# Kernel tuning notes

Measured on AMD Instinct MI355X. Metric: run time of the kernel, lower is better.

## Reference

```python
import jax, jax.numpy as jnp
import numpy as np

N, P, E, IN = 50000, 4, 500000, 128   # nodes, metapaths, edges/metapath, in_size
H, F = 8, 32                           # num_heads, out_feats per head (hidden_size)
HF = H * F                             # flattened embedding (256)
HS = 128                               # semantic attention hidden size
B, OUT = 128, 2                        # num contracts (graphs), classes
NEG_SLOPE = 0.2                        # DGL GATConv LeakyReLU slope


def setup_inputs() -> dict:
    key = jax.random.key(0)
    ks = jax.random.split(key, 14)
    return {
        "h": jax.random.normal(ks[0], (N, IN), jnp.float32),
        "Wg": jax.random.normal(ks[1], (P, IN, HF), jnp.float32) * 0.1,
        "attn_l": jax.random.normal(ks[2], (P, H, F), jnp.float32) * 0.1,
        "attn_r": jax.random.normal(ks[3], (P, H, F), jnp.float32) * 0.1,
        "gat_bias": jax.random.normal(ks[4], (P, HF), jnp.float32) * 0.1,
        "sem_W1": jax.random.normal(ks[5], (HF, HS), jnp.float32) * 0.1,
        "sem_b1": jax.random.normal(ks[6], (HS,), jnp.float32) * 0.1,
        "sem_W2": jax.random.normal(ks[7], (HS, 1), jnp.float32) * 0.1,
        "cls_W": jax.random.normal(ks[8], (HF, OUT), jnp.float32) * 0.1,
        "cls_b": jax.random.normal(ks[9], (OUT,), jnp.float32) * 0.1,
        "src": jax.random.randint(ks[10], (P, E), 0, N, jnp.int32),
        "dst": jax.random.randint(ks[11], (P, E), 0, N, jnp.int32),
        "graph_ids": jax.random.randint(ks[12], (N,), 0, B, jnp.int32),
    }


def _gat(h, W, al, ar, bias, s, d):
    """One DGL-style GATConv over an edge list (dropout=identity, eval mode)."""
    n = h.shape[0]
    hp = (h @ W).reshape(n, H, F)                 # [N,H,F] projected features
    el = (hp * al).sum(-1)                        # [N,H] src attention term
    er = (hp * ar).sum(-1)                        # [N,H] dst attention term
    e = jax.nn.leaky_relu(el[s] + er[d], NEG_SLOPE)        # [E,H] edge scores
    m = jax.ops.segment_max(e, d, num_segments=n)          # per-dst max (softmax stab.)
    a = jnp.exp(e - m[d])                                  # [E,H]
    den = jax.ops.segment_sum(a, d, num_segments=n)        # [N,H]
    alpha = a / den[d]                                     # edge softmax over in-neighbors
    out = jax.ops.segment_sum(alpha[:, :, None] * hp[s], d, num_segments=n)  # [N,H,F]
    return jax.nn.elu(out + bias.reshape(1, H, F)).reshape(n, HF)


def reference(h, Wg, attn_l, attn_r, gat_bias, sem_W1, sem_b1, sem_W2,
              cls_W, cls_b, src, dst, graph_ids):
    n = h.shape[0]
    # GATConv per meta-path (small fixed loop over P=4 metapaths)
    embs = [_gat(h, Wg[p], attn_l[p], attn_r[p], gat_bias[p], src[p], dst[p])
            for p in range(Wg.shape[0])]
    z = jnp.stack(embs, axis=1)                   # [N,P,HF]
    # Semantic attention over meta-paths
    w = jnp.tanh(z @ sem_W1 + sem_b1) @ sem_W2    # [N,P,1]
    beta = jax.nn.softmax(w.mean(0), axis=0)      # [P,1]
    fused = (beta[None] * z).sum(1)               # [N,HF]
    # Per-graph (filename) mean pooling
    seg = jax.ops.segment_sum(fused, graph_ids, num_segments=B)
    cnt = jax.ops.segment_sum(jnp.ones((n,), fused.dtype), graph_ids, num_segments=B)
    pooled = seg / jnp.maximum(cnt, 1.0)[:, None]  # [B,HF]
    logits = pooled @ cls_W + cls_b                # [B,OUT]
    return (logits, pooled)
```

## Files before the change

### kernel.cpp

```cpp
#include <hip/hip_runtime.h>

#define NN 50000
#define PM 4
#define EE 500000
#define INF_ 128
#define NH 8
#define FF 32
#define HF 256
#define HS 128
#define BG 128
#define OUTC 2

#define NB2 98
#define BCAP 6144
#define BCH 4096
#define GCAP 576
#define NBG2 782

typedef __attribute__((ext_vector_type(8))) short bf16x8;
typedef __attribute__((ext_vector_type(4))) float f32x4;

__device__ __forceinline__ float b2f(unsigned short x) {
  unsigned u = ((unsigned)x) << 16;
  return __builtin_bit_cast(float, u);
}
__device__ __forceinline__ unsigned short f2b(float f) {
  unsigned u = __builtin_bit_cast(unsigned, f);
  u += 0x7fff + ((u >> 16) & 1);
  return (unsigned short)(u >> 16);
}
__device__ __forceinline__ float fexp(float x) { return __expf(x); }
__device__ __forceinline__ float ftanh(float x) {
  float t = __expf(-2.f * fabsf(x));
  float r = (1.f - t) / (1.f + t);
  return copysignf(r, x);
}

__global__ __launch_bounds__(256) void prep_kernel(
    const float* __restrict__ h, const float* __restrict__ Wg,
    const float* __restrict__ W1, const float* __restrict__ al,
    const float* __restrict__ ar,
    unsigned short* __restrict__ h_b, unsigned short* __restrict__ Wb_t,
    unsigned short* __restrict__ W1_t, float* __restrict__ wl,
    float* __restrict__ wr, int* __restrict__ gcnt, int* __restrict__ gcnt2) {
  int b = blockIdx.x;
  int tid = threadIdx.x;
  if (b < 1) {
    for (int i = tid; i < PM * NB2; i += 256) gcnt[i] = 0;
    if (tid < BG) gcnt2[tid] = 0;
    return;
  }
  b -= 1;
  if (b < 6250) {
    int t = b * 256 + tid;
    float4 v = *(const float4*)(h + (size_t)t * 4);
    ushort4 o;
    o.x = f2b(v.x); o.y = f2b(v.y); o.z = f2b(v.z); o.w = f2b(v.w);
    *(ushort4*)(h_b + (size_t)t * 4) = o;
    return;
  }
  b -= 6250;
  if (b < 512) {
    int t = b * 256 + tid;
    int p = t >> 15, rem = t & 32767;
    int n = rem >> 7, k = rem & 127;
    Wb_t[(size_t)p * 32768 + n * 128 + k] = f2b(Wg[(size_t)p * 32768 + k * 256 + n]);
    return;
  }
  b -= 512;
  if (b < 128) {
    int t = b * 256 + tid;
    int n = t >> 8, k = t & 255;
    W1_t[n * 256 + k] = f2b(W1[k * 128 + n]);
    return;
  }
  b -= 128;
  {
    int t = b * 256 + tid;
    int p = t >> 10, rem = t & 1023;
    int k = rem >> 3, hh = rem & 7;
    const float* wrow = Wg + (size_t)p * 32768 + k * 256 + hh * 32;
    const float* alp = al + p * 256 + hh * 32;
    const float* arp = ar + p * 256 + hh * 32;
    float sl = 0.f, sr = 0.f;
    #pragma unroll
    for (int f = 0; f < 32; f++) { sl += wrow[f] * alp[f]; sr += wrow[f] * arp[f]; }
    wl[t] = sl; wr[t] = sr;
  }
}

__global__ __launch_bounds__(256) void bucket_kernel(
    const int* __restrict__ src, const int* __restrict__ dst,
    unsigned* __restrict__ bdata, int* __restrict__ gcnt) {
  __shared__ unsigned ed[BCH];
  __shared__ int hist[NB2], gbase[NB2], cur[NB2];
  int p = blockIdx.y;
  int e0 = blockIdx.x * BCH;
  int n = min(BCH, EE - e0);
  int tid = threadIdx.x;
  if (tid < NB2) hist[tid] = 0;
  __syncthreads();
  const int* sp = src + (size_t)p * EE + e0;
  const int* dp = dst + (size_t)p * EE + e0;
  for (int i = tid; i < n; i += 256) {
    int s = sp[i], d = dp[i];
    ed[i] = ((unsigned)d << 16) | (unsigned)s;
    atomicAdd(&hist[d >> 9], 1);
  }
  __syncthreads();
  if (tid < NB2) {
    gbase[tid] = atomicAdd(&gcnt[p * NB2 + tid], hist[tid]);
    cur[tid] = 0;
  }
  __syncthreads();
  for (int i = tid; i < n; i += 256) {
    unsigned pk = ed[i];
    int bk = pk >> 25;
    int slot = gbase[bk] + atomicAdd(&cur[bk], 1);
    if (slot < BCAP)
      bdata[((size_t)(p * NB2 + bk)) * BCAP + slot] = pk;
  }
}

__global__ __launch_bounds__(256) void gbucket_kernel(
    const int* __restrict__ gid, int* __restrict__ glist, int* __restrict__ gcnt2) {
  __shared__ int gl[BCH];
  __shared__ int hist[BG], gbase[BG], cur[BG];
  int e0 = blockIdx.x * BCH;
  int n = min(BCH, NN - e0);
  int tid = threadIdx.x;
  if (tid < BG) hist[tid] = 0;
  __syncthreads();
  for (int i = tid; i < n; i += 256) {
    int g = gid[e0 + i];
    gl[i] = g;
    atomicAdd(&hist[g], 1);
  }
  __syncthreads();
  if (tid < BG) {
    gbase[tid] = atomicAdd(&gcnt2[tid], hist[tid]);
    cur[tid] = 0;
  }
  __syncthreads();
  for (int i = tid; i < n; i += 256) {
    int g = gl[i];
    int slot = gbase[g] + atomicAdd(&cur[g], 1);
    if (slot < GCAP) glist[g * GCAP + slot] = e0 + i;
  }
}

__global__ __launch_bounds__(256) void csrify_kernel(
    const unsigned* __restrict__ bdata, const int* __restrict__ gcnt,
    int* __restrict__ off, unsigned short* __restrict__ csr) {
  __shared__ unsigned ebuf[BCAP];
  __shared__ int gc[NB2];
  __shared__ int degc[512];
  __shared__ int loff[513];
  __shared__ int tmp[256];
  __shared__ int base_s;
  int b = blockIdx.x, p = blockIdx.y;
  int tid = threadIdx.x;
  if (tid < NB2) gc[tid] = min(gcnt[p * NB2 + tid], BCAP);
  __syncthreads();
  if (tid == 0) {
    int s = 0;
    for (int i = 0; i < b; i++) s += gc[i];
    base_s = s;
  }
  int cnt = gc[b];
  const unsigned* bp = bdata + ((size_t)(p * NB2 + b)) * BCAP;
  for (int i = tid; i < cnt; i += 256) ebuf[i] = bp[i];
  degc[tid] = 0; degc[256 + tid] = 0;
  __syncthreads();
  for (int i = tid; i < cnt; i += 256)
    atomicAdd(&degc[(ebuf[i] >> 16) & 511], 1);
  __syncthreads();
  int d0 = degc[2 * tid], d1 = degc[2 * tid + 1];
  tmp[tid] = d0 + d1;
  __syncthreads();
  for (int o = 1; o < 256; o <<= 1) {
    int v = (tid >= o) ? tmp[tid - o] : 0;
    __syncthreads();
    tmp[tid] += v;
    __syncthreads();
  }
  int bse = tmp[tid] - d0 - d1;
  loff[2 * tid] = bse; loff[2 * tid + 1] = bse + d0;
  if (tid == 255) loff[512] = tmp[255];
  __syncthreads();
  int base = base_s;
  for (int dl = tid; dl < 512; dl += 256) {
    int n = b * 512 + dl;
    if (n <= NN) off[(size_t)p * (NN + 1) + n] = base + loff[dl];
  }
  degc[tid] = 0; degc[256 + tid] = 0;
  __syncthreads();
  for (int i = tid; i < cnt; i += 256) {
    unsigned pk = ebuf[i];
    int dl = (pk >> 16) & 511;
    int slot = loff[dl] + atomicAdd(&degc[dl], 1);
    csr[(size_t)p * EE + base + slot] = (unsigned short)(pk & 0xffff);
  }
}

__global__ __launch_bounds__(256) void gemm1_kernel(
    const unsigned short* __restrict__ hA, const unsigned short* __restrict__ Bt,
    unsigned short* __restrict__ Cb, int M, int p0, size_t cstride) {
  __shared__ unsigned short As[64 * 128];
  __shared__ unsigned short Bs[128 * 128];
  int tid = threadIdx.x;
  int pl = blockIdx.z;
  const unsigned short* Bp = Bt + (size_t)(p0 + pl) * 32768;
  unsigned short* Cp = Cb + (size_t)pl * cstride;
  int row0 = blockIdx.x * 64, col0 = blockIdx.y * 128;
  #pragma unroll
  for (int i = 0; i < 4; i++) {
    int c = i * 256 + tid;
    int row = c >> 4, g = c & 15;
    int grow = row0 + row;
    uint4 v = make_uint4(0, 0, 0, 0);
    if (grow < M) v = *(const uint4*)(hA + (size_t)grow * 128 + g * 8);
    *(uint4*)&As[row * 128 + ((g ^ (row & 15)) << 3)] = v;
  }
  #pragma unroll
  for (int i = 0; i < 8; i++) {
    int c = i * 256 + tid;
    int row = c >> 4, g = c & 15;
    uint4 v = *(const uint4*)(Bp + (size_t)(col0 + row) * 128 + g * 8);
    *(uint4*)&Bs[row * 128 + ((g ^ (row & 15)) << 3)] = v;
  }
  __syncthreads();
  int wave = tid >> 6, lane = tid & 63;
  int ln = lane & 15, quad = lane >> 4;
  int mbase = (wave >> 1) * 32, nbase = (wave & 1) * 64;
  f32x4 acc[2][4] = {};
  #pragma unroll
  for (int ks = 0; ks < 4; ks++) {
    int g = ks * 4 + quad;
    bf16x8 a[2], bb[4];
    #pragma unroll
    for (int mi = 0; mi < 2; mi++) {
      int r = mbase + mi * 16 + ln;
      a[mi] = *(const bf16x8*)&As[r * 128 + ((g ^ ln) << 3)];
    }
    #pragma unroll
    for (int ni = 0; ni < 4; ni++) {
      int r = nbase + ni * 16 + ln;
      bb[ni] = *(const bf16x8*)&Bs[r * 128 + ((g ^ ln) << 3)];
    }
    #pragma unroll
    for (int mi = 0; mi < 2; mi++)
      #pragma unroll
      for (int ni = 0; ni < 4; ni++)
        acc[mi][ni] = __builtin_amdgcn_mfma_f32_16x16x32_bf16(a[mi], bb[ni], acc[mi][ni], 0, 0, 0);
  }
  #pragma unroll
  for (int mi = 0; mi < 2; mi++) {
    int gm0 = row0 + mbase + mi * 16 + quad * 4;
    #pragma unroll
    for (int ni = 0; ni < 4; ni++) {
      int gn = col0 + nbase + ni * 16 + ln;
      #pragma unroll
      for (int r = 0; r < 4; r++) {
        int gm = gm0 + r;
        if (gm < M) Cp[(size_t)gm * 256 + gn] = f2b(acc[mi][ni][r]);
      }
    }
  }
}

__global__ __launch_bounds__(256) void elr_kernel(
    const unsigned short* __restrict__ h_b, const float* __restrict__ wl,
    const float* __restrict__ wr, float* __restrict__ el,
    float* __restrict__ er, int N, int p0, size_t estride) {
  __shared__ float wls[128 * 8], wrs[128 * 8];
  int pl = blockIdx.y;
  const float* wlp = wl + (size_t)(p0 + pl) * 1024;
  const float* wrp = wr + (size_t)(p0 + pl) * 1024;
  float* elp = el + (size_t)pl * estride;
  float* erp = er + (size_t)pl * estride;
  for (int i = threadIdx.x; i < 1024; i += 256) { wls[i] = wlp[i]; wrs[i] = wrp[i]; }
  __syncthreads();
  int n = blockIdx.x * 256 + threadIdx.x;
  if (n >= N) return;
  float accl[8] = {}, accr[8] = {};
  for (int kk = 0; kk < 16; kk++) {
    uint4 raw = *(const uint4*)(h_b + (size_t)n * 128 + kk * 8);
    unsigned uu[4] = {raw.x, raw.y, raw.z, raw.w};
    #pragma unroll
    for (int q = 0; q < 4; q++) {
      float v0 = __builtin_bit_cast(float, uu[q] << 16);
      float v1 = __builtin_bit_cast(float, uu[q] & 0xffff0000u);
      int k = kk * 8 + q * 2;
      #pragma unroll
      for (int hh = 0; hh < 8; hh++) {
        accl[hh] += v0 * wls[k * 8 + hh] + v1 * wls[(k + 1) * 8 + hh];
        accr[hh] += v0 * wrs[k * 8 + hh] + v1 * wrs[(k + 1) * 8 + hh];
      }
    }
  }
  *(float4*)(elp + (size_t)n * 8)     = make_float4(accl[0], accl[1], accl[2], accl[3]);
  *(float4*)(elp + (size_t)n * 8 + 4) = make_float4(accl[4], accl[5], accl[6], accl[7]);
  *(float4*)(erp + (size_t)n * 8)     = make_float4(accr[0], accr[1], accr[2], accr[3]);
  *(float4*)(erp + (size_t)n * 8 + 4) = make_float4(accr[4], accr[5], accr[6], accr[7]);
}

__global__ __launch_bounds__(256) void agg_kernel(
    const unsigned short* __restrict__ hp_b, const float* __restrict__ el,
    const float* __restrict__ er, const unsigned short* __restrict__ csr,
    const int* __restrict__ off, const float* __restrict__ bias,
    unsigned short* __restrict__ emb_b, int N, int p0,
    size_t hstride, size_t estride, size_t embstride) {
  int pl = blockIdx.y;
  int p = p0 + pl;
  const unsigned short* hp = hp_b + (size_t)pl * hstride;
  const float* elp = el + (size_t)pl * estride;
  const float* erp = er + (size_t)pl * estride;
  const unsigned short* csrp = csr + (size_t)p * EE;
  const int* offp = off + (size_t)p * (NN + 1);
  const float* bp = bias + (size_t)p * HF;
  unsigned short* embp = emb_b + (size_t)pl * embstride;
  int n = blockIdx.x * 4 + (threadIdx.x >> 6);
  if (n >= N) return;
  int lane = threadIdx.x & 63;
  int h = lane >> 3;
  int e0 = offp[n], e1 = offp[n + 1];
  float erh = erp[n * NH + h];
  float den = 0.f, a0 = 0.f, a1 = 0.f, a2 = 0.f, a3 = 0.f;
  int e = e0;
  for (; e + 8 <= e1; e += 8) {
    int s[8];
    #pragma unroll
    for (int j = 0; j < 8; j++) s[j] = csrp[e + j];
    float x[8];
    #pragma unroll
    for (int j = 0; j < 8; j++) x[j] = elp[s[j] * NH + h];
    ushort4 hv[8];
    #pragma unroll
    for (int j = 0; j < 8; j++)
      hv[j] = *(const ushort4*)(hp + (size_t)s[j] * HF + lane * 4);
    float w[8];
    #pragma unroll
    for (int j = 0; j < 8; j++) {
      float xx = x[j] + erh;
      xx = fmaxf(xx, 0.2f * xx);
      w[j] = fexp(xx);
    }
    den += ((w[0] + w[1]) + (w[2] + w[3])) + ((w[4] + w[5]) + (w[6] + w[7]));
    a0 += ((w[0] * b2f(hv[0].x) + w[1] * b2f(hv[1].x)) + (w[2] * b2f(hv[2].x) + w[3] * b2f(hv[3].x)))
        + ((w[4] * b2f(hv[4].x) + w[5] * b2f(hv[5].x)) + (w[6] * b2f(hv[6].x) + w[7] * b2f(hv[7].x)));
    a1 += ((w[0] * b2f(hv[0].y) + w[1] * b2f(hv[1].y)) + (w[2] * b2f(hv[2].y) + w[3] * b2f(hv[3].y)))
        + ((w[4] * b2f(hv[4].y) + w[5] * b2f(hv[5].y)) + (w[6] * b2f(hv[6].y) + w[7] * b2f(hv[7].y)));
    a2 += ((w[0] * b2f(hv[0].z) + w[1] * b2f(hv[1].z)) + (w[2] * b2f(hv[2].z) + w[3] * b2f(hv[3].z)))
        + ((w[4] * b2f(hv[4].z) + w[5] * b2f(hv[5].z)) + (w[6] * b2f(hv[6].z) + w[7] * b2f(hv[7].z)));
    a3 += ((w[0] * b2f(hv[0].w) + w[1] * b2f(hv[1].w)) + (w[2] * b2f(hv[2].w) + w[3] * b2f(hv[3].w)))
        + ((w[4] * b2f(hv[4].w) + w[5] * b2f(hv[5].w)) + (w[6] * b2f(hv[6].w) + w[7] * b2f(hv[7].w)));
  }
  if (e + 4 <= e1) {
    int s0 = csrp[e], s1 = csrp[e + 1], s2 = csrp[e + 2], s3 = csrp[e + 3];
    float x0 = elp[s0 * NH + h] + erh;
    float x1 = elp[s1 * NH + h] + erh;
    float x2 = elp[s2 * NH + h] + erh;
    float x3 = elp[s3 * NH + h] + erh;
    ushort4 h0 = *(const ushort4*)(hp + (size_t)s0 * HF + lane * 4);
    ushort4 h1 = *(const ushort4*)(hp + (size_t)s1 * HF + lane * 4);
    ushort4 h2 = *(const ushort4*)(hp + (size_t)s2 * HF + lane * 4);
    ushort4 h3 = *(const ushort4*)(hp + (size_t)s3 * HF + lane * 4);
    x0 = fmaxf(x0, 0.2f * x0); x1 = fmaxf(x1, 0.2f * x1);
    x2 = fmaxf(x2, 0.2f * x2); x3 = fmaxf(x3, 0.2f * x3);
    float w0 = fexp(x0), w1 = fexp(x1), w2 = fexp(x2), w3 = fexp(x3);
    den += (w0 + w1) + (w2 + w3);
    a0 += (w0 * b2f(h0.x) + w1 * b2f(h1.x)) + (w2 * b2f(h2.x) + w3 * b2f(h3.x));
    a1 += (w0 * b2f(h0.y) + w1 * b2f(h1.y)) + (w2 * b2f(h2.y) + w3 * b2f(h3.y));
    a2 += (w0 * b2f(h0.z) + w1 * b2f(h1.z)) + (w2 * b2f(h2.z) + w3 * b2f(h3.z));
    a3 += (w0 * b2f(h0.w) + w1 * b2f(h1.w)) + (w2 * b2f(h2.w) + w3 * b2f(h3.w));
    e += 4;
  }
  for (; e < e1; e++) {
    int s = csrp[e];
    float x = elp[s * NH + h] + erh;
    x = fmaxf(x, 0.2f * x);
    float w = fexp(x);
    den += w;
    ushort4 hv = *(const ushort4*)(hp + (size_t)s * HF + lane * 4);
    a0 += w * b2f(hv.x); a1 += w * b2f(hv.y);
    a2 += w * b2f(hv.z); a3 += w * b2f(hv.w);
  }
  float inv = (den > 0.f) ? 1.f / den : 0.f;
  float4 bv = *(const float4*)(bp + lane * 4);
  float o0 = a0 * inv + bv.x, o1 = a1 * inv + bv.y;
  float o2 = a2 * inv + bv.z, o3 = a3 * inv + bv.w;
  o0 = (o0 > 0.f) ? o0 : fexp(o0) - 1.f;
  o1 = (o1 > 0.f) ? o1 : fexp(o1) - 1.f;
  o2 = (o2 > 0.f) ? o2 : fexp(o2) - 1.f;
  o3 = (o3 > 0.f) ? o3 : fexp(o3) - 1.f;
  ushort4 ov;
  ov.x = f2b(o0); ov.y = f2b(o1); ov.z = f2b(o2); ov.w = f2b(o3);
  *(ushort4*)(embp + (size_t)n * HF + lane * 4) = ov;
}

__global__ __launch_bounds__(256) void gemm2_kernel(
    const unsigned short* __restrict__ A, const unsigned short* __restrict__ Bt,
    const float* __restrict__ b1, const float* __restrict__ W2,
    float* __restrict__ wpart, int M, int p0, size_t astride) {
  __shared__ unsigned short As[64 * 128];
  __shared__ unsigned short Bs[128 * 128];
  __shared__ float wred[4];
  int tid = threadIdx.x;
  int pl = blockIdx.y;
  const unsigned short* Ap = A + (size_t)pl * astride;
  int row0 = blockIdx.x * 64;
  int wave = tid >> 6, lane = tid & 63;
  int ln = lane & 15, quad = lane >> 4;
  int mbase = (wave >> 1) * 32, nbase = (wave & 1) * 64;
  f32x4 acc[2][4] = {};
  for (int kc = 0; kc < 2; kc++) {
    #pragma unroll
    for (int i = 0; i < 4; i++) {
      int c = i * 256 + tid;
      int row = c >> 4, g = c & 15;
      int grow = row0 + row;
      uint4 v = make_uint4(0, 0, 0, 0);
      if (grow < M) v = *(const uint4*)(Ap + (size_t)grow * 256 + kc * 128 + g * 8);
      *(uint4*)&As[row * 128 + ((g ^ (row & 15)) << 3)] = v;
    }
    #pragma unroll
    for (int i = 0; i < 8; i++) {
      int c = i * 256 + tid;
      int row = c >> 4, g = c & 15;
      uint4 v = *(const uint4*)(Bt + (size_t)row * 256 + kc * 128 + g * 8);
      *(uint4*)&Bs[row * 128 + ((g ^ (row & 15)) << 3)] = v;
    }
    __syncthreads();
    #pragma unroll
    for (int ks = 0; ks < 4; ks++) {
      int g = ks * 4 + quad;
      bf16x8 a[2], bb[4];
      #pragma unroll
      for (int mi = 0; mi < 2; mi++) {
        int r = mbase + mi * 16 + ln;
        a[mi] = *(const bf16x8*)&As[r * 128 + ((g ^ ln) << 3)];
      }
      #pragma unroll
      for (int ni = 0; ni < 4; ni++) {
        int r = nbase + ni * 16 + ln;
        bb[ni] = *(const bf16x8*)&Bs[r * 128 + ((g ^ ln) << 3)];
      }
      #pragma unroll
      for (int mi = 0; mi < 2; mi++)
        #pragma unroll
        for (int ni = 0; ni < 4; ni++)
          acc[mi][ni] = __builtin_amdgcn_mfma_f32_16x16x32_bf16(a[mi], bb[ni], acc[mi][ni], 0, 0, 0);
    }
    __syncthreads();
  }
  float b1v[4], w2v[4];
  #pragma unroll
  for (int ni = 0; ni < 4; ni++) {
    int col = nbase + ni * 16 + ln;
    b1v[ni] = b1[col]; w2v[ni] = W2[col];
  }
  float s = 0.f;
  #pragma unroll
  for (int mi = 0; mi < 2; mi++) {
    int gm0 = row0 + mbase + mi * 16 + quad * 4;
    #pragma unroll
    for (int r = 0; r < 4; r++) {
      if (gm0 + r < M) {
        #pragma unroll
        for (int ni = 0; ni < 4; ni++)
          s += ftanh(acc[mi][ni][r] + b1v[ni]) * w2v[ni];
      }
    }
  }
  #pragma unroll
  for (int o = 32; o > 0; o >>= 1) s += __shfl_down(s, o);
  if (lane == 0) wred[wave] = s;
  __syncthreads();
  if (tid == 0)
    wpart[(size_t)(p0 + pl) * NBG2 + blockIdx.x] =
        (wred[0] + wred[1]) + (wred[2] + wred[3]);
}

__global__ __launch_bounds__(256) void pool_kernel(
    const unsigned short* __restrict__ emb, const int* __restrict__ glist,
    const int* __restrict__ gcnt2, float* __restrict__ pool,
    int p0, size_t embstride) {
  __shared__ int nl[GCAP];
  __shared__ float sm[4][64][4];
  int b = blockIdx.x, pl = blockIdx.y;
  const unsigned short* embp = emb + (size_t)pl * embstride;
  int tid = threadIdx.x;
  int cnt = min(gcnt2[b], GCAP);
  for (int i = tid; i < cnt; i += 256) nl[i] = glist[b * GCAP + i];
  __syncthreads();
  int sub = tid >> 6, lane = tid & 63;
  float a0 = 0.f, a1 = 0.f, a2 = 0.f, a3 = 0.f;
  for (int i = sub; i < cnt; i += 4) {
    ushort4 v = *(const ushort4*)(embp + (size_t)nl[i] * HF + lane * 4);
    a0 += b2f(v.x); a1 += b2f(v.y); a2 += b2f(v.z); a3 += b2f(v.w);
  }
  sm[sub][lane][0] = a0; sm[sub][lane][1] = a1;
  sm[sub][lane][2] = a2; sm[sub][lane][3] = a3;
  __syncthreads();
  int fl = tid >> 2, j = tid & 3;
  float s = sm[0][fl][j] + sm[1][fl][j] + sm[2][fl][j] + sm[3][fl][j];
  pool[((size_t)(p0 + pl) * BG + b) * HF + tid] = s;
}

__global__ __launch_bounds__(256) void final_kernel(
    const float* __restrict__ pool, const float* __restrict__ wpart,
    const int* __restrict__ gcnt2, const float* __restrict__ clsW,
    const float* __restrict__ clsb, float* __restrict__ out, int N) {
  int b = blockIdx.x;
  int f = threadIdx.x;
  __shared__ float red[256];
  float wm[PM];
  #pragma unroll
  for (int p = 0; p < PM; p++) {
    float s = 0.f;
    for (int i = f; i < NBG2; i += 256) s += wpart[(size_t)p * NBG2 + i];
    red[f] = s;
    __syncthreads();
    for (int st = 128; st > 0; st >>= 1) {
      if (f < st) red[f] += red[f + st];
      __syncthreads();
    }
    wm[p] = red[0] / (float)N;
    __syncthreads();
  }
  float c = fmaxf((float)gcnt2[b], 1.f);
  float mx = -1e30f;
  #pragma unroll
  for (int p = 0; p < PM; p++) mx = fmaxf(mx, wm[p]);
  float es = 0.f, e[PM];
  #pragma unroll
  for (int p = 0; p < PM; p++) { e[p] = expf(wm[p] - mx); es += e[p]; }
  float v = 0.f;
  #pragma unroll
  for (int p = 0; p < PM; p++)
    v += (e[p] / es) * pool[((size_t)p * BG + b) * HF + f];
  v /= c;
  out[256 + (size_t)b * HF + f] = v;
  __shared__ float sm[256];
  sm[f] = v * clsW[f * 2 + 0];
  __syncthreads();
  for (int st = 128; st > 0; st >>= 1) {
    if (f < st) sm[f] += sm[f + st];
    __syncthreads();
  }
  float l0 = sm[0];
  __syncthreads();
  sm[f] = v * clsW[f * 2 + 1];
  __syncthreads();
  for (int st = 128; st > 0; st >>= 1) {
    if (f < st) sm[f] += sm[f + st];
    __syncthreads();
  }
  if (f == 0) {
    out[b * 2 + 0] = l0 + clsb[0];
    out[b * 2 + 1] = sm[0] + clsb[1];
  }
}

extern "C" void kernel_launch(void* const* d_in, const int* in_sizes, int n_in,
                              void* d_out, int out_size, void* d_ws, size_t ws_size,
                              hipStream_t stream) {
  const float* h      = (const float*)d_in[0];
  const float* Wg     = (const float*)d_in[1];
  const float* attn_l = (const float*)d_in[2];
  const float* attn_r = (const float*)d_in[3];
  const float* gatb   = (const float*)d_in[4];
  const float* semW1  = (const float*)d_in[5];
  const float* semb1  = (const float*)d_in[6];
  const float* semW2  = (const float*)d_in[7];
  const float* clsW   = (const float*)d_in[8];
  const float* clsb   = (const float*)d_in[9];
  const int*   src    = (const int*)d_in[10];
  const int*   dst    = (const int*)d_in[11];
  const int*   gid    = (const int*)d_in[12];
  float* out = (float*)d_out;

  auto layout_size = [](int PMg) -> size_t {
    size_t o = 0;
    auto alloc = [&](size_t bytes) { o += (bytes + 255) & ~(size_t)255; };
    alloc((size_t)NN * INF_ * 2);
    alloc((size_t)PMg * NN * HF * 2);
    alloc((size_t)PMg * NN * HF * 2);
    alloc((size_t)PM * HF * INF_ * 2);
    alloc((size_t)HS * HF * 2);
    alloc((size_t)PM * INF_ * NH * 4);
    alloc((size_t)PM * INF_ * NH * 4);
    alloc((size_t)PMg * NN * NH * 4);
    alloc((size_t)PMg * NN * NH * 4);
    alloc((size_t)PM * NB2 * BCAP * 4);
    alloc((size_t)PM * NB2 * 4);
    alloc((size_t)BG * GCAP * 4);
    alloc((size_t)BG * 4);
    alloc((size_t)PM * (NN + 1) * 4);
    alloc((size_t)PM * EE * 2);
    alloc((size_t)PM * BG * HF * 4);
    alloc((size_t)PM * NBG2 * 4);
    return o;
  };
  int PMg = (layout_size(4) <= ws_size) ? 4 : 1;

  char* ws = (char*)d_ws;
  size_t o = 0;
  auto alloc = [&](size_t bytes) { size_t r = o; o += (bytes + 255) & ~(size_t)255; return r; };
  unsigned short* h_b   = (unsigned short*)(ws + alloc((size_t)NN * INF_ * 2));
  unsigned short* hp_b  = (unsigned short*)(ws + alloc((size_t)PMg * NN * HF * 2));
  unsigned short* emb_b = (unsigned short*)(ws + alloc((size_t)PMg * NN * HF * 2));
  unsigned short* Wb_t  = (unsigned short*)(ws + alloc((size_t)PM * HF * INF_ * 2));
  unsigned short* W1_t  = (unsigned short*)(ws + alloc((size_t)HS * HF * 2));
  float* wl    = (float*)(ws + alloc((size_t)PM * INF_ * NH * 4));
  float* wr    = (float*)(ws + alloc((size_t)PM * INF_ * NH * 4));
  float* el    = (float*)(ws + alloc((size_t)PMg * NN * NH * 4));
  float* er    = (float*)(ws + alloc((size_t)PMg * NN * NH * 4));
  unsigned* bdata = (unsigned*)(ws + alloc((size_t)PM * NB2 * BCAP * 4));
  int*   gcnt  = (int*)(ws + alloc((size_t)PM * NB2 * 4));
  int*   glist = (int*)(ws + alloc((size_t)BG * GCAP * 4));
  int*   gcnt2 = (int*)(ws + alloc((size_t)BG * 4));
  int*   off   = (int*)(ws + alloc((size_t)PM * (NN + 1) * 4));
  unsigned short* csr = (unsigned short*)(ws + alloc((size_t)PM * EE * 2));
  float* pool  = (float*)(ws + alloc((size_t)PM * BG * HF * 4));
  float* wpart = (float*)(ws + alloc((size_t)PM * NBG2 * 4));

  const size_t hpS  = (PMg == 4) ? (size_t)NN * HF : 0;
  const size_t embS = hpS;
  const size_t elS  = (PMg == 4) ? (size_t)NN * NH : 0;

  prep_kernel<<<1 + 6250 + 512 + 128 + 16, 256, 0, stream>>>(
      h, Wg, semW1, attn_l, attn_r, h_b, Wb_t, W1_t, wl, wr, gcnt, gcnt2);
  bucket_kernel<<<dim3((EE + BCH - 1) / BCH, PM), 256, 0, stream>>>(src, dst, bdata, gcnt);
  gbucket_kernel<<<(NN + BCH - 1) / BCH, 256, 0, stream>>>(gid, glist, gcnt2);
  csrify_kernel<<<dim3(NB2, PM), 256, 0, stream>>>(bdata, gcnt, off, csr);

  if (PMg == 4) {
    gemm1_kernel<<<dim3((NN + 63) / 64, 2, 4), 256, 0, stream>>>(h_b, Wb_t, hp_b, NN, 0, hpS);
    elr_kernel<<<dim3((NN + 255) / 256, 4), 256, 0, stream>>>(h_b, wl, wr, el, er, NN, 0, elS);
    agg_kernel<<<dim3((NN + 3) / 4, 4), 256, 0, stream>>>(
        hp_b, el, er, csr, off, gatb, emb_b, NN, 0, hpS, elS, embS);
    gemm2_kernel<<<dim3(NBG2, 4), 256, 0, stream>>>(
        emb_b, W1_t, semb1, semW2, wpart, NN, 0, embS);
    pool_kernel<<<dim3(BG, 4), 256, 0, stream>>>(emb_b, glist, gcnt2, pool, 0, embS);
  } else {
    for (int p = 0; p < PM; p++) {
      gemm1_kernel<<<dim3((NN + 63) / 64, 2, 1), 256, 0, stream>>>(h_b, Wb_t, hp_b, NN, p, 0);
      elr_kernel<<<dim3((NN + 255) / 256, 1), 256, 0, stream>>>(h_b, wl, wr, el, er, NN, p, 0);
      agg_kernel<<<dim3((NN + 3) / 4, 1), 256, 0, stream>>>(
          hp_b, el, er, csr, off, gatb, emb_b, NN, p, 0, 0, 0);
      gemm2_kernel<<<dim3(NBG2, 1), 256, 0, stream>>>(
          emb_b, W1_t, semb1, semW2, wpart, NN, p, 0);
      pool_kernel<<<dim3(BG, 1), 256, 0, stream>>>(emb_b, glist, gcnt2, pool, p, 0);
    }
  }

  final_kernel<<<BG, 256, 0, stream>>>(pool, wpart, gcnt2, clsW, clsb, out, NN);
}
```

Before: 457.2 us.

## Merge independent kernels into combined launches and reuse A fragments across metapaths

Merges independent kernel pairs into single launches, with each block choosing its role from its block index: edge bucketing with graph bucketing, GEMM1 with the el/er projection, and GEMM2 with pooling. The GEMM1 blocks now loop over all metapaths, loading the h tile and its MFMA A fragments once and reusing them, instead of using a z grid dimension. This removes several launch gaps, lets the small kernels fill idle compute units, and cuts repeated A loads. In exchange, GEMM1 has fewer blocks each doing more sequential work, and the shared shared-memory size may limit occupancy for the lighter roles.

```diff
diff --git a/kernel.cpp b/kernel.cpp
--- a/kernel.cpp
+++ b/kernel.cpp
@@ -14,7 +14,11 @@
 #define NB2 98
 #define BCAP 6144
 #define BCH 4096
+#define NBB 123
+#define NGB 13
 #define GCAP 576
+#define NBG1 782
+#define NBE 196
 #define NBG2 782
 
 typedef __attribute__((ext_vector_type(8))) short bf16x8;
@@ -89,63 +93,70 @@
   }
 }
 
-__global__ __launch_bounds__(256) void bucket_kernel(
+__global__ __launch_bounds__(256) void bg_kernel(
     const int* __restrict__ src, const int* __restrict__ dst,
-    unsigned* __restrict__ bdata, int* __restrict__ gcnt) {
-  __shared__ unsigned ed[BCH];
-  __shared__ int hist[NB2], gbase[NB2], cur[NB2];
-  int p = blockIdx.y;
-  int e0 = blockIdx.x * BCH;
-  int n = min(BCH, EE - e0);
+    unsigned* __restrict__ bdata, int* __restrict__ gcnt,
+    const int* __restrict__ gid, int* __restrict__ glist,
+    int* __restrict__ gcnt2) {
+  __shared__ __align__(16) char smem[18432];
+  int b = blockIdx.x;
   int tid = threadIdx.x;
-  if (tid < NB2) hist[tid] = 0;
-  __syncthreads();
-  const int* sp = src + (size_t)p * EE + e0;
-  const int* dp = dst + (size_t)p * EE + e0;
-  for (int i = tid; i < n; i += 256) {
-    int s = sp[i], d = dp[i];
-    ed[i] = ((unsigned)d << 16) | (unsigned)s;
-    atomicAdd(&hist[d >> 9], 1);
-  }
-  __syncthreads();
-  if (tid < NB2) {
-    gbase[tid] = atomicAdd(&gcnt[p * NB2 + tid], hist[tid]);
-    cur[tid] = 0;
-  }
-  __syncthreads();
-  for (int i = tid; i < n; i += 256) {
-    unsigned pk = ed[i];
-    int bk = pk >> 25;
-    int slot = gbase[bk] + atomicAdd(&cur[bk], 1);
-    if (slot < BCAP)
-      bdata[((size_t)(p * NB2 + bk)) * BCAP + slot] = pk;
-  }
-}
-
-__global__ __launch_bounds__(256) void gbucket_kernel(
-    const int* __restrict__ gid, int* __restrict__ glist, int* __restrict__ gcnt2) {
-  __shared__ int gl[BCH];
-  __shared__ int hist[BG], gbase[BG], cur[BG];
-  int e0 = blockIdx.x * BCH;
-  int n = min(BCH, NN - e0);
-  int tid = threadIdx.x;
-  if (tid < BG) hist[tid] = 0;
-  __syncthreads();
-  for (int i = tid; i < n; i += 256) {
-    int g = gid[e0 + i];
-    gl[i] = g;
-    atomicAdd(&hist[g], 1);
-  }
-  __syncthreads();
-  if (tid < BG) {
-    gbase[tid] = atomicAdd(&gcnt2[tid], hist[tid]);
-    cur[tid] = 0;
-  }
-  __syncthreads();
-  for (int i = tid; i < n; i += 256) {
-    int g = gl[i];
-    int slot = gbase[g] + atomicAdd(&cur[g], 1);
-    if (slot < GCAP) glist[g * GCAP + slot] = e0 + i;
+  if (b < NBB * PM) {
+    unsigned* ed = (unsigned*)smem;
+    int* hist  = (int*)(smem + BCH * 4);
+    int* gbase = hist + NB2;
+    int* cur   = gbase + NB2;
+    int p = b / NBB, blk = b % NBB;
+    int e0 = blk * BCH;
+    int n = min(BCH, EE - e0);
+    if (tid < NB2) hist[tid] = 0;
+    __syncthreads();
+    const int* sp = src + (size_t)p * EE + e0;
+    const int* dp = dst + (size_t)p * EE + e0;
+    for (int i = tid; i < n; i += 256) {
+      int s = sp[i], d = dp[i];
+      ed[i] = ((unsigned)d << 16) | (unsigned)s;
+      atomicAdd(&hist[d >> 9], 1);
+    }
+    __syncthreads();
+    if (tid < NB2) {
+      gbase[tid] = atomicAdd(&gcnt[p * NB2 + tid], hist[tid]);
+      cur[tid] = 0;
+    }
+    __syncthreads();
+    for (int i = tid; i < n; i += 256) {
+      unsigned pk = ed[i];
+      int bk = pk >> 25;
+      int slot = gbase[bk] + atomicAdd(&cur[bk], 1);
+      if (slot < BCAP)
+        bdata[((size_t)(p * NB2 + bk)) * BCAP + slot] = pk;
+    }
+  } else {
+    int* gl    = (int*)smem;
+    int* hist  = (int*)(smem + BCH * 4);
+    int* gbase = hist + BG;
+    int* cur   = gbase + BG;
+    int blk = b - NBB * PM;
+    int e0 = blk * BCH;
+    int n = min(BCH, NN - e0);
+    if (tid < BG) hist[tid] = 0;
+    __syncthreads();
+    for (int i = tid; i < n; i += 256) {
+      int g = gid[e0 + i];
+      gl[i] = g;
+      atomicAdd(&hist[g], 1);
+    }
+    __syncthreads();
+    if (tid < BG) {
+      gbase[tid] = atomicAdd(&gcnt2[tid], hist[tid]);
+      cur[tid] = 0;
+    }
+    __syncthreads();
+    for (int i = tid; i < n; i += 256) {
+      int g = gl[i];
+      int slot = gbase[g] + atomicAdd(&cur[g], 1);
+      if (slot < GCAP) glist[g * GCAP + slot] = e0 + i;
+    }
   }
 }
 
@@ -203,106 +214,121 @@
   }
 }
 
-__global__ __launch_bounds__(256) void gemm1_kernel(
+__global__ __launch_bounds__(256) void g1elr_kernel(
     const unsigned short* __restrict__ hA, const unsigned short* __restrict__ Bt,
-    unsigned short* __restrict__ Cb, int M, int p0, size_t cstride) {
-  __shared__ unsigned short As[64 * 128];
-  __shared__ unsigned short Bs[128 * 128];
+    unsigned short* __restrict__ Cb, const float* __restrict__ wl,
+    const float* __restrict__ wr, float* __restrict__ el, float* __restrict__ er,
+    int M, int p0, int npaths, size_t cstride, size_t estride) {
+  __shared__ __align__(16) char smem[49152];
+  int b = blockIdx.x;
   int tid = threadIdx.x;
-  int pl = blockIdx.z;
-  const unsigned short* Bp = Bt + (size_t)(p0 + pl) * 32768;
-  unsigned short* Cp = Cb + (size_t)pl * cstride;
-  int row0 = blockIdx.x * 64, col0 = blockIdx.y * 128;
-  #pragma unroll
-  for (int i = 0; i < 4; i++) {
-    int c = i * 256 + tid;
-    int row = c >> 4, g = c & 15;
-    int grow = row0 + row;
-    uint4 v = make_uint4(0, 0, 0, 0);
-    if (grow < M) v = *(const uint4*)(hA + (size_t)grow * 128 + g * 8);
-    *(uint4*)&As[row * 128 + ((g ^ (row & 15)) << 3)] = v;
-  }
-  #pragma unroll
-  for (int i = 0; i < 8; i++) {
-    int c = i * 256 + tid;
-    int row = c >> 4, g = c & 15;
-    uint4 v = *(const uint4*)(Bp + (size_t)(col0 + row) * 128 + g * 8);
-    *(uint4*)&Bs[row * 128 + ((g ^ (row & 15)) << 3)] = v;
-  }
-  __syncthreads();
-  int wave = tid >> 6, lane = tid & 63;
-  int ln = lane & 15, quad = lane >> 4;
-  int mbase = (wave >> 1) * 32, nbase = (wave & 1) * 64;
-  f32x4 acc[2][4] = {};
-  #pragma unroll
-  for (int ks = 0; ks < 4; ks++) {
-    int g = ks * 4 + quad;
-    bf16x8 a[2], bb[4];
-    #pragma unroll
-    for (int mi = 0; mi < 2; mi++) {
-      int r = mbase + mi * 16 + ln;
-      a[mi] = *(const bf16x8*)&As[r * 128 + ((g ^ ln) << 3)];
-    }
-    #pragma unroll
-    for (int ni = 0; ni < 4; ni++) {
-      int r = nbase + ni * 16 + ln;
-      bb[ni] = *(const bf16x8*)&Bs[r * 128 + ((g ^ ln) << 3)];
-    }
-    #pragma unroll
-    for (int mi = 0; mi < 2; mi++)
-      #pragma unroll
-      for (int ni = 0; ni < 4; ni++)
-        acc[mi][ni] = __builtin_amdgcn_mfma_f32_16x16x32_bf16(a[mi], bb[ni], acc[mi][ni], 0, 0, 0);
-  }
-  #pragma unroll
-  for (int mi = 0; mi < 2; mi++) {
-    int gm0 = row0 + mbase + mi * 16 + quad * 4;
-    #pragma unroll
-    for (int ni = 0; ni < 4; ni++) {
-      int gn = col0 + nbase + ni * 16 + ln;
-      #pragma unroll
-      for (int r = 0; r < 4; r++) {
-        int gm = gm0 + r;
-        if (gm < M) Cp[(size_t)gm * 256 + gn] = f2b(acc[mi][ni][r]);
-      }
-    }
-  }
-}
-
-__global__ __launch_bounds__(256) void elr_kernel(
-    const unsigned short* __restrict__ h_b, const float* __restrict__ wl,
-    const float* __restrict__ wr, float* __restrict__ el,
-    float* __restrict__ er, int N, int p0, size_t estride) {
-  __shared__ float wls[128 * 8], wrs[128 * 8];
-  int pl = blockIdx.y;
-  const float* wlp = wl + (size_t)(p0 + pl) * 1024;
-  const float* wrp = wr + (size_t)(p0 + pl) * 1024;
-  float* elp = el + (size_t)pl * estride;
-  float* erp = er + (size_t)pl * estride;
-  for (int i = threadIdx.x; i < 1024; i += 256) { wls[i] = wlp[i]; wrs[i] = wrp[i]; }
-  __syncthreads();
-  int n = blockIdx.x * 256 + threadIdx.x;
-  if (n >= N) return;
-  float accl[8] = {}, accr[8] = {};
-  for (int kk = 0; kk < 16; kk++) {
-    uint4 raw = *(const uint4*)(h_b + (size_t)n * 128 + kk * 8);
-    unsigned uu[4] = {raw.x, raw.y, raw.z, raw.w};
-    #pragma unroll
-    for (int q = 0; q < 4; q++) {
-      float v0 = __builtin_bit_cast(float, uu[q] << 16);
-      float v1 = __builtin_bit_cast(float, uu[q] & 0xffff0000u);
-      int k = kk * 8 + q * 2;
-      #pragma unroll
-      for (int hh = 0; hh < 8; hh++) {
-        accl[hh] += v0 * wls[k * 8 + hh] + v1 * wls[(k + 1) * 8 + hh];
-        accr[hh] += v0 * wrs[k * 8 + hh] + v1 * wrs[(k + 1) * 8 + hh];
-      }
-    }
-  }
-  *(float4*)(elp + (size_t)n * 8)     = make_float4(accl[0], accl[1], accl[2], accl[3]);
-  *(float4*)(elp + (size_t)n * 8 + 4) = make_float4(accl[4], accl[5], accl[6], accl[7]);
-  *(float4*)(erp + (size_t)n * 8)     = make_float4(accr[0], accr[1], accr[2], accr[3]);
-  *(float4*)(erp + (size_t)n * 8 + 4) = make_float4(accr[4], accr[5], accr[6], accr[7]);
+  int nb1 = NBG1 * 2;
+  if (b < nb1) {
+    unsigned short* As = (unsigned short*)smem;
+    unsigned short* Bs = (unsigned short*)(smem + 16384);
+    int row0 = (b >> 1) * 64, col0 = (b & 1) * 128;
+    #pragma unroll
+    for (int i = 0; i < 4; i++) {
+      int c = i * 256 + tid;
+      int row = c >> 4, g = c & 15;
+      int grow = row0 + row;
+      uint4 v = make_uint4(0, 0, 0, 0);
+      if (grow < M) v = *(const uint4*)(hA + (size_t)grow * 128 + g * 8);
+      *(uint4*)&As[row * 128 + ((g ^ (row & 15)) << 3)] = v;
+    }
+    int wave = tid >> 6, lane = tid & 63;
+    int ln = lane & 15, quad = lane >> 4;
+    int mbase = (wave >> 1) * 32, nbase = (wave & 1) * 64;
+    bf16x8 afr[4][2];
+    bool afr_ok = false;
+    for (int pl = 0; pl < npaths; pl++) {
+      const unsigned short* Bp = Bt + (size_t)(p0 + pl) * 32768;
+      #pragma unroll
+      for (int i = 0; i < 8; i++) {
+        int c = i * 256 + tid;
+        int row = c >> 4, g = c & 15;
+        uint4 v = *(const uint4*)(Bp + (size_t)(col0 + row) * 128 + g * 8);
+        *(uint4*)&Bs[row * 128 + ((g ^ (row & 15)) << 3)] = v;
+      }
+      __syncthreads();
+      if (!afr_ok) {
+        #pragma unroll
+        for (int ks = 0; ks < 4; ks++) {
+          int g = ks * 4 + quad;
+          #pragma unroll
+          for (int mi = 0; mi < 2; mi++) {
+            int r = mbase + mi * 16 + ln;
+            afr[ks][mi] = *(const bf16x8*)&As[r * 128 + ((g ^ ln) << 3)];
+          }
+        }
+        afr_ok = true;
+      }
+      f32x4 acc[2][4] = {};
+      #pragma unroll
+      for (int ks = 0; ks < 4; ks++) {
+        int g = ks * 4 + quad;
+        bf16x8 bb[4];
+        #pragma unroll
+        for (int ni = 0; ni < 4; ni++) {
+          int r = nbase + ni * 16 + ln;
+          bb[ni] = *(const bf16x8*)&Bs[r * 128 + ((g ^ ln) << 3)];
+        }
+        #pragma unroll
+        for (int mi = 0; mi < 2; mi++)
+          #pragma unroll
+          for (int ni = 0; ni < 4; ni++)
+            acc[mi][ni] = __builtin_amdgcn_mfma_f32_16x16x32_bf16(afr[ks][mi], bb[ni], acc[mi][ni], 0, 0, 0);
+      }
+      unsigned short* Cp = Cb + (size_t)pl * cstride;
+      #pragma unroll
+      for (int mi = 0; mi < 2; mi++) {
+        int gm0 = row0 + mbase + mi * 16 + quad * 4;
+        #pragma unroll
+        for (int ni = 0; ni < 4; ni++) {
+          int gn = col0 + nbase + ni * 16 + ln;
+          #pragma unroll
+          for (int r = 0; r < 4; r++) {
+            int gm = gm0 + r;
+            if (gm < M) Cp[(size_t)gm * 256 + gn] = f2b(acc[mi][ni][r]);
+          }
+        }
+      }
+      __syncthreads();
+    }
+  } else {
+    float* wls = (float*)smem;
+    float* wrs = wls + 1024;
+    int t = b - nb1;
+    int pl = t / NBE, nblk = t % NBE;
+    const float* wlp = wl + (size_t)(p0 + pl) * 1024;
+    const float* wrp = wr + (size_t)(p0 + pl) * 1024;
+    float* elp = el + (size_t)pl * estride;
+    float* erp = er + (size_t)pl * estride;
+    for (int i = tid; i < 1024; i += 256) { wls[i] = wlp[i]; wrs[i] = wrp[i]; }
+    __syncthreads();
+    int n = nblk * 256 + tid;
+    if (n >= M) return;
+    float accl[8] = {}, accr[8] = {};
+    for (int kk = 0; kk < 16; kk++) {
+      uint4 raw = *(const uint4*)(hA + (size_t)n * 128 + kk * 8);
+      unsigned uu[4] = {raw.x, raw.y, raw.z, raw.w};
+      #pragma unroll
+      for (int q = 0; q < 4; q++) {
+        float v0 = __builtin_bit_cast(float, uu[q] << 16);
+        float v1 = __builtin_bit_cast(float, uu[q] & 0xffff0000u);
+        int k = kk * 8 + q * 2;
+        #pragma unroll
+        for (int hh = 0; hh < 8; hh++) {
+          accl[hh] += v0 * wls[k * 8 + hh] + v1 * wls[(k + 1) * 8 + hh];
+          accr[hh] += v0 * wrs[k * 8 + hh] + v1 * wrs[(k + 1) * 8 + hh];
+        }
+      }
+    }
+    *(float4*)(elp + (size_t)n * 8)     = make_float4(accl[0], accl[1], accl[2], accl[3]);
+    *(float4*)(elp + (size_t)n * 8 + 4) = make_float4(accl[4], accl[5], accl[6], accl[7]);
+    *(float4*)(erp + (size_t)n * 8)     = make_float4(accr[0], accr[1], accr[2], accr[3]);
+    *(float4*)(erp + (size_t)n * 8 + 4) = make_float4(accr[4], accr[5], accr[6], accr[7]);
+  }
 }
 
 __global__ __launch_bounds__(256) void agg_kernel(
@@ -399,113 +425,118 @@
   *(ushort4*)(embp + (size_t)n * HF + lane * 4) = ov;
 }
 
-__global__ __launch_bounds__(256) void gemm2_kernel(
+__global__ __launch_bounds__(256) void g2pool_kernel(
     const unsigned short* __restrict__ A, const unsigned short* __restrict__ Bt,
     const float* __restrict__ b1, const float* __restrict__ W2,
-    float* __restrict__ wpart, int M, int p0, size_t astride) {
-  __shared__ unsigned short As[64 * 128];
-  __shared__ unsigned short Bs[128 * 128];
-  __shared__ float wred[4];
+    float* __restrict__ wpart, const int* __restrict__ glist,
+    const int* __restrict__ gcnt2, float* __restrict__ pool,
+    int M, int p0, int npaths, size_t astride) {
+  __shared__ __align__(16) char smem[49168];
+  int b = blockIdx.x;
   int tid = threadIdx.x;
-  int pl = blockIdx.y;
-  const unsigned short* Ap = A + (size_t)pl * astride;
-  int row0 = blockIdx.x * 64;
-  int wave = tid >> 6, lane = tid & 63;
-  int ln = lane & 15, quad = lane >> 4;
-  int mbase = (wave >> 1) * 32, nbase = (wave & 1) * 64;
-  f32x4 acc[2][4] = {};
-  for (int kc = 0; kc < 2; kc++) {
-    #pragma unroll
-    for (int i = 0; i < 4; i++) {
-      int c = i * 256 + tid;
-      int row = c >> 4, g = c & 15;
-      int grow = row0 + row;
-      uint4 v = make_uint4(0, 0, 0, 0);
-      if (grow < M) v = *(const uint4*)(Ap + (size_t)grow * 256 + kc * 128 + g * 8);
-      *(uint4*)&As[row * 128 + ((g ^ (row & 15)) << 3)] = v;
-    }
-    #pragma unroll
-    for (int i = 0; i < 8; i++) {
-      int c = i * 256 + tid;
-      int row = c >> 4, g = c & 15;
-      uint4 v = *(const uint4*)(Bt + (size_t)row * 256 + kc * 128 + g * 8);
-      *(uint4*)&Bs[row * 128 + ((g ^ (row & 15)) << 3)] = v;
-    }
-    __syncthreads();
-    #pragma unroll
-    for (int ks = 0; ks < 4; ks++) {
-      int g = ks * 4 + quad;
-      bf16x8 a[2], bb[4];
-      #pragma unroll
-      for (int mi = 0; mi < 2; mi++) {
-        int r = mbase + mi * 16 + ln;
-        a[mi] = *(const bf16x8*)&As[r * 128 + ((g ^ ln) << 3)];
-      }
-      #pragma unroll
-      for (int ni = 0; ni < 4; ni++) {
-        int r = nbase + ni * 16 + ln;
-        bb[ni] = *(const bf16x8*)&Bs[r * 128 + ((g ^ ln) << 3)];
-      }
-      #pragma unroll
-      for (int mi = 0; mi < 2; mi++)
-        #pragma unroll
-        for (int ni = 0; ni < 4; ni++)
-          acc[mi][ni] = __builtin_amdgcn_mfma_f32_16x16x32_bf16(a[mi], bb[ni], acc[mi][ni], 0, 0, 0);
-    }
-    __syncthreads();
-  }
-  float b1v[4], w2v[4];
-  #pragma unroll
-  for (int ni = 0; ni < 4; ni++) {
-    int col = nbase + ni * 16 + ln;
-    b1v[ni] = b1[col]; w2v[ni] = W2[col];
-  }
-  float s = 0.f;
-  #pragma unroll
-  for (int mi = 0; mi < 2; mi++) {
-    int gm0 = row0 + mbase + mi * 16 + quad * 4;
-    #pragma unroll
-    for (int r = 0; r < 4; r++) {
-      if (gm0 + r < M) {
-        #pragma unroll
-        for (int ni = 0; ni < 4; ni++)
-          s += ftanh(acc[mi][ni][r] + b1v[ni]) * w2v[ni];
-      }
-    }
-  }
-  #pragma unroll
-  for (int o = 32; o > 0; o >>= 1) s += __shfl_down(s, o);
-  if (lane == 0) wred[wave] = s;
-  __syncthreads();
-  if (tid == 0)
-    wpart[(size_t)(p0 + pl) * NBG2 + blockIdx.x] =
-        (wred[0] + wred[1]) + (wred[2] + wred[3]);
-}
-
-__global__ __launch_bounds__(256) void pool_kernel(
-    const unsigned short* __restrict__ emb, const int* __restrict__ glist,
-    const int* __restrict__ gcnt2, float* __restrict__ pool,
-    int p0, size_t embstride) {
-  __shared__ int nl[GCAP];
-  __shared__ float sm[4][64][4];
-  int b = blockIdx.x, pl = blockIdx.y;
-  const unsigned short* embp = emb + (size_t)pl * embstride;
-  int tid = threadIdx.x;
-  int cnt = min(gcnt2[b], GCAP);
-  for (int i = tid; i < cnt; i += 256) nl[i] = glist[b * GCAP + i];
-  __syncthreads();
-  int sub = tid >> 6, lane = tid & 63;
-  float a0 = 0.f, a1 = 0.f, a2 = 0.f, a3 = 0.f;
-  for (int i = sub; i < cnt; i += 4) {
-    ushort4 v = *(const ushort4*)(embp + (size_t)nl[i] * HF + lane * 4);
-    a0 += b2f(v.x); a1 += b2f(v.y); a2 += b2f(v.z); a3 += b2f(v.w);
-  }
-  sm[sub][lane][0] = a0; sm[sub][lane][1] = a1;
-  sm[sub][lane][2] = a2; sm[sub][lane][3] = a3;
-  __syncthreads();
-  int fl = tid >> 2, j = tid & 3;
-  float s = sm[0][fl][j] + sm[1][fl][j] + sm[2][fl][j] + sm[3][fl][j];
-  pool[((size_t)(p0 + pl) * BG + b) * HF + tid] = s;
+  int nb2 = NBG2 * npaths;
+  if (b < nb2) {
+    unsigned short* As = (unsigned short*)smem;
+    unsigned short* Bs = (unsigned short*)(smem + 16384);
+    float* wred = (float*)(smem + 49152);
+    int bx = b % NBG2, pl = b / NBG2;
+    const unsigned short* Ap = A + (size_t)pl * astride;
+    int row0 = bx * 64;
+    int wave = tid >> 6, lane = tid & 63;
+    int ln = lane & 15, quad = lane >> 4;
+    int mbase = (wave >> 1) * 32, nbase = (wave & 1) * 64;
+    f32x4 acc[2][4] = {};
+    for (int kc = 0; kc < 2; kc++) {
+      #pragma unroll
+      for (int i = 0; i < 4; i++) {
+        int c = i * 256 + tid;
+        int row = c >> 4, g = c & 15;
+        int grow = row0 + row;
+        uint4 v = make_uint4(0, 0, 0, 0);
+        if (grow < M) v = *(const uint4*)(Ap + (size_t)grow * 256 + kc * 128 + g * 8);
+        *(uint4*)&As[row * 128 + ((g ^ (row & 15)) << 3)] = v;
+      }
+      #pragma unroll
+      for (int i = 0; i < 8; i++) {
+        int c = i * 256 + tid;
+        int row = c >> 4, g = c & 15;
+        uint4 v = *(const uint4*)(Bt + (size_t)row * 256 + kc * 128 + g * 8);
+        *(uint4*)&Bs[row * 128 + ((g ^ (row & 15)) << 3)] = v;
+      }
+      __syncthreads();
+      #pragma unroll
+      for (int ks = 0; ks < 4; ks++) {
+        int g = ks * 4 + quad;
+        bf16x8 a[2], bb[4];
+        #pragma unroll
+        for (int mi = 0; mi < 2; mi++) {
+          int r = mbase + mi * 16 + ln;
+          a[mi] = *(const bf16x8*)&As[r * 128 + ((g ^ ln) << 3)];
+        }
+        #pragma unroll
+        for (int ni = 0; ni < 4; ni++) {
+          int r = nbase + ni * 16 + ln;
+          bb[ni] = *(const bf16x8*)&Bs[r * 128 + ((g ^ ln) << 3)];
+        }
+        #pragma unroll
+        for (int mi = 0; mi < 2; mi++)
+          #pragma unroll
+          for (int ni = 0; ni < 4; ni++)
+            acc[mi][ni] = __builtin_amdgcn_mfma_f32_16x16x32_bf16(a[mi], bb[ni], acc[mi][ni], 0, 0, 0);
+      }
+      __syncthreads();
+    }
+    float b1v[4], w2v[4];
+    #pragma unroll
+    for (int ni = 0; ni < 4; ni++) {
+      int col = nbase + ni * 16 + ln;
+      b1v[ni] = b1[col]; w2v[ni] = W2[col];
+    }
+    float s = 0.f;
+    #pragma unroll
+    for (int mi = 0; mi < 2; mi++) {
+      int gm0 = row0 + mbase + mi * 16 + quad * 4;
+      #pragma unroll
+      for (int r = 0; r < 4; r++) {
+        if (gm0 + r < M) {
+          #pragma unroll
+          for (int ni = 0; ni < 4; ni++)
+            s += ftanh(acc[mi][ni][r] + b1v[ni]) * w2v[ni];
+        }
+      }
+    }
+    #pragma unroll
+    for (int o = 32; o > 0; o >>= 1) s += __shfl_down(s, o);
+    if (lane == 0) wred[wave] = s;
+    __syncthreads();
+    if (tid == 0)
+      wpart[(size_t)(p0 + pl) * NBG2 + bx] =
+          (wred[0] + wred[1]) + (wred[2] + wred[3]);
+  } else {
+    int* nl = (int*)smem;
+    float* sm = (float*)(smem + GCAP * 4);
+    int i0 = b - nb2;
+    int g = i0 % BG, pl = i0 / BG;
+    const unsigned short* embp = A + (size_t)pl * astride;
+    int cnt = min(gcnt2[g], GCAP);
+    for (int i = tid; i < cnt; i += 256) nl[i] = glist[g * GCAP + i];
+    __syncthreads();
+    int sub = tid >> 6, lane = tid & 63;
+    float a0 = 0.f, a1 = 0.f, a2 = 0.f, a3 = 0.f;
+    for (int i = sub; i < cnt; i += 4) {
+      ushort4 v = *(const ushort4*)(embp + (size_t)nl[i] * HF + lane * 4);
+      a0 += b2f(v.x); a1 += b2f(v.y); a2 += b2f(v.z); a3 += b2f(v.w);
+    }
+    sm[(sub * 64 + lane) * 4 + 0] = a0;
+    sm[(sub * 64 + lane) * 4 + 1] = a1;
+    sm[(sub * 64 + lane) * 4 + 2] = a2;
+    sm[(sub * 64 + lane) * 4 + 3] = a3;
+    __syncthreads();
+    int fl = tid >> 2, j = tid & 3;
+    float s = sm[(0 * 64 + fl) * 4 + j] + sm[(1 * 64 + fl) * 4 + j]
+            + sm[(2 * 64 + fl) * 4 + j] + sm[(3 * 64 + fl) * 4 + j];
+    pool[((size_t)(p0 + pl) * BG + g) * HF + tid] = s;
+  }
 }
 
 __global__ __launch_bounds__(256) void final_kernel(
@@ -632,27 +663,24 @@
 
   prep_kernel<<<1 + 6250 + 512 + 128 + 16, 256, 0, stream>>>(
       h, Wg, semW1, attn_l, attn_r, h_b, Wb_t, W1_t, wl, wr, gcnt, gcnt2);
-  bucket_kernel<<<dim3((EE + BCH - 1) / BCH, PM), 256, 0, stream>>>(src, dst, bdata, gcnt);
-  gbucket_kernel<<<(NN + BCH - 1) / BCH, 256, 0, stream>>>(gid, glist, gcnt2);
+  bg_kernel<<<NBB * PM + NGB, 256, 0, stream>>>(src, dst, bdata, gcnt, gid, glist, gcnt2);
   csrify_kernel<<<dim3(NB2, PM), 256, 0, stream>>>(bdata, gcnt, off, csr);
 
   if (PMg == 4) {
-    gemm1_kernel<<<dim3((NN + 63) / 64, 2, 4), 256, 0, stream>>>(h_b, Wb_t, hp_b, NN, 0, hpS);
-    elr_kernel<<<dim3((NN + 255) / 256, 4), 256, 0, stream>>>(h_b, wl, wr, el, er, NN, 0, elS);
+    g1elr_kernel<<<NBG1 * 2 + NBE * 4, 256, 0, stream>>>(
+        h_b, Wb_t, hp_b, wl, wr, el, er, NN, 0, 4, hpS, elS);
     agg_kernel<<<dim3((NN + 3) / 4, 4), 256, 0, stream>>>(
         hp_b, el, er, csr, off, gatb, emb_b, NN, 0, hpS, elS, embS);
-    gemm2_kernel<<<dim3(NBG2, 4), 256, 0, stream>>>(
-        emb_b, W1_t, semb1, semW2, wpart, NN, 0, embS);
-    pool_kernel<<<dim3(BG, 4), 256, 0, stream>>>(emb_b, glist, gcnt2, pool, 0, embS);
+    g2pool_kernel<<<NBG2 * 4 + BG * 4, 256, 0, stream>>>(
+        emb_b, W1_t, semb1, semW2, wpart, glist, gcnt2, pool, NN, 0, 4, embS);
   } else {
     for (int p = 0; p < PM; p++) {
-      gemm1_kernel<<<dim3((NN + 63) / 64, 2, 1), 256, 0, stream>>>(h_b, Wb_t, hp_b, NN, p, 0);
-      elr_kernel<<<dim3((NN + 255) / 256, 1), 256, 0, stream>>>(h_b, wl, wr, el, er, NN, p, 0);
+      g1elr_kernel<<<NBG1 * 2 + NBE, 256, 0, stream>>>(
+          h_b, Wb_t, hp_b, wl, wr, el, er, NN, p, 1, 0, 0);
       agg_kernel<<<dim3((NN + 3) / 4, 1), 256, 0, stream>>>(
           hp_b, el, er, csr, off, gatb, emb_b, NN, p, 0, 0, 0);
-      gemm2_kernel<<<dim3(NBG2, 1), 256, 0, stream>>>(
-          emb_b, W1_t, semb1, semW2, wpart, NN, p, 0);
-      pool_kernel<<<dim3(BG, 1), 256, 0, stream>>>(emb_b, glist, gcnt2, pool, p, 0);
+      g2pool_kernel<<<NBG2 + BG, 256, 0, stream>>>(
+          emb_b, W1_t, semb1, semW2, wpart, glist, gcnt2, pool, NN, p, 1, 0);
     }
   }
 
```

New measurement: 432.3 us. 5.5% less time.
